# Kernel tuning notes

Measured on AMD Instinct MI355X. Metric: run time of the kernel, lower is better.

The kernel has to match this reference:

```python
import jax, jax.numpy as jnp
import numpy as np

COMMIT_WEIGHT = 0.25


def setup_inputs() -> dict:
    key = jax.random.key(0)
    k1, k2 = jax.random.split(key)
    B, D, T, K = 8, 512, 2048, 8192
    x = jax.random.normal(k1, (B, D, T), dtype=jnp.float32)
    codebook = jax.random.normal(k2, (K, D), dtype=jnp.float32)
    return {"x": x, "codebook": codebook}


def reference(x, codebook):
    # x: [B, D, T] channels-first; VQ operates on [B, T, D]
    xt = jnp.transpose(x, (0, 2, 1))  # [B, T, D]
    x2 = jnp.sum(xt * xt, axis=-1, keepdims=True)          # [B, T, 1]
    e2 = jnp.sum(codebook * codebook, axis=-1)             # [K]
    xe = jnp.einsum('btd,kd->btk', xt, codebook)           # [B, T, K] (dominant GEMM)
    dists = x2 - 2.0 * xe + e2                             # [B, T, K]
    indices = jnp.argmin(dists, axis=-1)                   # [B, T] int
    quantized = codebook[indices]                          # [B, T, D] gather
    # commitment loss: ||sg(q) - x||^2 mean
    commit_loss = COMMIT_WEIGHT * jnp.mean(
        (jax.lax.stop_gradient(quantized) - xt) ** 2)
    # straight-through estimator
    quantized = xt + jax.lax.stop_gradient(quantized - xt)
    quantized = jnp.transpose(quantized, (0, 2, 1))        # back to [B, D, T]
    return quantized, indices, commit_loss
```

## Files before the change

kernel.cpp:

```cpp
#include <hip/hip_runtime.h>
#include <cstdint>
#include <cstddef>

#define B_   8
#define D_   512
#define T_   2048
#define K_   8192
#define BT_  (B_ * T_)
#define NQ_  ((size_t)B_ * D_ * T_)

typedef _Float16 f16x8 __attribute__((ext_vector_type(8)));
typedef _Float16 f16x4 __attribute__((ext_vector_type(4)));
typedef float    f32x4 __attribute__((ext_vector_type(4)));
typedef unsigned long long u64;
typedef unsigned int u32;

#define WS_SLOTS_OFF    0
#define WS_FIDX_OFF     393216
#define WS_PART_OFF     458752
#define WS_E2_OFF       460800
#define WS_XH_OFF       524288
#define WS_XL_OFF       (WS_XH_OFF + 16777216)
#define WS_CH_OFF       (WS_XL_OFF + 16777216)
#define WS_NEEDED       ((size_t)WS_CH_OFF + 8388608)

__device__ __forceinline__ void gload_lds16(const void* g, void* l) {
    __builtin_amdgcn_global_load_lds(
        (const __attribute__((address_space(1))) void*)g,
        (__attribute__((address_space(3))) void*)l, 16, 0, 0);
}

__device__ __forceinline__ u32 fkey(float f) {
    u32 u = __float_as_uint(f);
    u ^= (u32)((int)u >> 31) | 0x80000000u;
    return u;
}
__device__ __forceinline__ u64 umin64(u64 a, u64 b) { return a < b ? a : b; }
__device__ __forceinline__ u64 umax64(u64 a, u64 b) { return a > b ? a : b; }

__global__ __launch_bounds__(256) void k_prepcb(const float* __restrict__ cb,
                                                _Float16* __restrict__ ch,
                                                float* __restrict__ e2) {
    const int wid = threadIdx.x >> 6, lane = threadIdx.x & 63;
    const int row = blockIdx.x * 4 + wid;
    const float4* src = (const float4*)(cb + (size_t)row * D_ + lane * 8);
    float4 a = src[0], b = src[1];
    f16x8 h;
    h[0] = (_Float16)a.x; h[1] = (_Float16)a.y;
    h[2] = (_Float16)a.z; h[3] = (_Float16)a.w;
    h[4] = (_Float16)b.x; h[5] = (_Float16)b.y;
    h[6] = (_Float16)b.z; h[7] = (_Float16)b.w;
    *(f16x8*)(ch + (size_t)row * D_ + lane * 8) = h;
    float s = a.x * a.x;
    s = fmaf(a.y, a.y, s); s = fmaf(a.z, a.z, s); s = fmaf(a.w, a.w, s);
    s = fmaf(b.x, b.x, s); s = fmaf(b.y, b.y, s);
    s = fmaf(b.z, b.z, s); s = fmaf(b.w, b.w, s);
#pragma unroll
    for (int st = 1; st < 64; st <<= 1) s += __shfl_xor(s, st);
    if (lane == 0) e2[row] = s;
}

__global__ __launch_bounds__(256) void k_e2(const float* __restrict__ cb,
                                            float* __restrict__ e2) {
    int k = blockIdx.x * 256 + threadIdx.x;
    const float4* row = (const float4*)(cb + (size_t)k * D_);
    float s = 0.f;
#pragma unroll 4
    for (int i = 0; i < D_ / 4; ++i) {
        float4 v = row[i];
        s = fmaf(v.x, v.x, s); s = fmaf(v.y, v.y, s);
        s = fmaf(v.z, v.z, s); s = fmaf(v.w, v.w, s);
    }
    e2[k] = s;
}

__global__ __launch_bounds__(256) void k_splitx(const float* __restrict__ x,
                                                _Float16* __restrict__ xh,
                                                _Float16* __restrict__ xl) {
    int b  = blockIdx.z;
    int d0 = blockIdx.y * 64;
    int t0 = blockIdx.x * 64;
    int dl = threadIdx.x & 63;
    int tq = threadIdx.x >> 6;
    const float* px = x + ((size_t)b * D_ + (d0 + dl)) * T_ + t0 + tq * 16;
#pragma unroll
    for (int i = 0; i < 4; ++i) {
        float4 v = *(const float4*)(px + i * 4);
#pragma unroll
        for (int j = 0; j < 4; ++j) {
            float vv = (j == 0) ? v.x : (j == 1) ? v.y : (j == 2) ? v.z : v.w;
            _Float16 h = (_Float16)vv;
            float lo = vv - (float)h;
            _Float16 l = (_Float16)lo;
            size_t row = (size_t)b * T_ + t0 + tq * 16 + i * 4 + j;
            xh[row * D_ + d0 + dl] = h;
            xl[row * D_ + d0 + dl] = l;
        }
    }
}

__global__ __launch_bounds__(512, 2)
void k_hi_argmin(const _Float16* __restrict__ xh, const _Float16* __restrict__ ch,
                 const float* __restrict__ e2, u64* __restrict__ slots) {
    __shared__ char smem[131072];
    __shared__ u32 stop[256][2][2];
    __shared__ float e2s[1024];

    const int tid = threadIdx.x;
    const int xcd = blockIdx.x & 7;
    const int bi  = blockIdx.x >> 3;
    const int m_  = bi >> 3;
    const int nblk = bi & 7;
    const int mbase  = (xcd * 8 + m_) * 256;
    const int nstart = nblk * 1024;

    const int lane = tid & 63;
    const int wid  = tid >> 6;
    const int wr = wid & 3, wc = wid >> 2;
    const int lr = lane & 15, lg = lane >> 4;

    {
        u32* p = (u32*)stop;
        p[tid] = ~0u; p[tid + 512] = ~0u;
        *(float2*)&e2s[tid * 2] = *(const float2*)&e2[nstart + tid * 2];
    }
    __syncthreads();

    const bool isA = wid < 4;
    const int q8 = lane >> 3;
    const int u8 = (lane & 7) ^ q8;
    const int srow2 = (u8 >> 2) & 1;
    const int sslot = u8 & 3;
    const char* gs0 = isA
        ? (const char*)xh + (size_t)(mbase  + (wid & 3) * 64 + 2 * q8 + srow2) * 1024
              + sslot * 16
        : (const char*)ch + (size_t)(nstart + (wid & 3) * 64 + 2 * q8 + srow2) * 1024
              + sslot * 16;
    const int ldsbase = (isA ? 0 : 16384) + (wid & 3) * 4096;

#define STAGE2(g, i0) do {                                                   \
        char* lb_ = smem + ((g) & 3) * 32768 + ldsbase;                      \
        const char* gs_ = gs0 + (isA ? 0 : (size_t)((g) >> 4) * 262144)      \
                          + ((g) & 15) * 64;                                 \
        gload_lds16(gs_ + (size_t)(i0) * 16384, lb_ + (i0) * 1024);          \
        gload_lds16(gs_ + (size_t)((i0) + 1) * 16384, lb_ + ((i0) + 1) * 1024); \
    } while (0)

    const int lrh = lr >> 1;
    const int swz16 = ((lg + 4 * (lr & 1)) ^ lrh) * 16;
    const int aoff0 = (wr * 32 + lrh) * 128 + swz16;
    const int boff0 = 16384 + (wc * 64 + lrh) * 128 + swz16;

    u32 top2a[16], top2b[16];
#pragma unroll
    for (int s = 0; s < 16; ++s) { top2a[s] = ~0u; top2b[s] = ~0u; }

    f32x4 acc[4][8];
#pragma unroll
    for (int m = 0; m < 4; ++m)
#pragma unroll
        for (int n = 0; n < 8; ++n)
            acc[m][n] = (f32x4){0.f, 0.f, 0.f, 0.f};

    auto epilogue = [&](int ns) {
        float e2v[8];
#pragma unroll
        for (int n = 0; n < 8; ++n)
            e2v[n] = 0.5f * e2s[ns * 256 + wc * 128 + n * 16 + lr];
        const u32 base10 = ((u32)ns << 8) | ((u32)wc << 7) | (u32)lr;
#pragma unroll
        for (int m = 0; m < 4; ++m) {
#pragma unroll
            for (int j = 0; j < 4; ++j) {
                const int s = m * 4 + j;
                u32 t1 = top2a[s], t2 = top2b[s];
#pragma unroll
                for (int n = 0; n < 8; ++n) {
                    float d = fmaxf(e2v[n] - acc[m][n][j], 1.0f);
                    u32 p = (__float_as_uint(d) & 0xFFFFFC00u) | (base10 + ((u32)n << 4));
                    u32 mx = t1 > p ? t1 : p;
                    t1 = t1 < p ? t1 : p;
                    t2 = t2 < mx ? t2 : mx;
                }
                top2a[s] = t1; top2b[s] = t2;
            }
        }
#pragma unroll
        for (int m = 0; m < 4; ++m)
#pragma unroll
            for (int n = 0; n < 8; ++n)
                acc[m][n] = (f32x4){0.f, 0.f, 0.f, 0.f};
    };

#define MFMA16(AF, BF, NOFF)                                                 \
        __builtin_amdgcn_s_setprio(1);                                       \
        _Pragma("unroll")                                                    \
        for (int m = 0; m < 4; ++m)                                          \
            _Pragma("unroll")                                                \
            for (int n = 0; n < 4; ++n)                                      \
                acc[m][(NOFF) + n] = __builtin_amdgcn_mfma_f32_16x16x32_f16( \
                    AF[m], BF[n], acc[m][(NOFF) + n], 0, 0, 0);              \
        __builtin_amdgcn_s_setprio(0);

#define SB __builtin_amdgcn_sched_barrier(0)

    STAGE2(0, 0); STAGE2(0, 2);
    STAGE2(1, 0); STAGE2(1, 2);
    STAGE2(2, 0); STAGE2(2, 2);
    asm volatile("s_waitcnt vmcnt(8)" ::: "memory");
    __builtin_amdgcn_s_barrier();
    SB;

#pragma unroll 1
    for (int s = 0; s < 64; ++s) {
        const char* base = smem + (s & 3) * 32768;
        f16x8 af[4], bf[4], bg[4];

#pragma unroll
        for (int m = 0; m < 4; ++m)
            af[m] = *(const f16x8*)(base + aoff0 + m * 1024);
#pragma unroll
        for (int n = 0; n < 4; ++n)
            bf[n] = *(const f16x8*)(base + boff0 + n * 1024);
        if (s < 61) STAGE2(s + 3, 0);
        SB;
        MFMA16(af, bf, 0)
        SB;
#pragma unroll
        for (int n = 0; n < 4; ++n)
            bg[n] = *(const f16x8*)(base + boff0 + (4 + n) * 1024);
        if (s < 61) STAGE2(s + 3, 2);
        SB;
        MFMA16(af, bg, 4)
        SB;

        if (s < 61)       asm volatile("s_waitcnt vmcnt(8)" ::: "memory");
        else if (s == 61) asm volatile("s_waitcnt vmcnt(4)" ::: "memory");
        else              asm volatile("s_waitcnt vmcnt(0)" ::: "memory");
        asm volatile("s_waitcnt lgkmcnt(0)" ::: "memory");
        SB;
        __builtin_amdgcn_s_barrier();
        SB;
        if ((s & 15) == 15) epilogue(s >> 4);
    }
#undef STAGE2
#undef MFMA16
#undef SB

#pragma unroll
    for (int m = 0; m < 4; ++m) {
#pragma unroll
        for (int j = 0; j < 4; ++j) {
            const int s = m * 4 + j;
            u32 t1 = top2a[s], t2 = top2b[s];
#pragma unroll
            for (int st = 1; st < 16; st <<= 1) {
                u32 o1 = __shfl_xor(t1, st);
                u32 o2 = __shfl_xor(t2, st);
                u32 mx = t1 > o1 ? t1 : o1;
                u32 sel = t1 < o1 ? t2 : o2;
                u32 n2 = mx < sel ? mx : sel;
                t1 = t1 < o1 ? t1 : o1;
                t2 = t2 < n2 ? t2 : n2;
            }
            if (lr == 0) {
                int ql = wr * 64 + m * 16 + lg * 4 + j;
                stop[ql][wc][0] = t1; stop[ql][wc][1] = t2;
            }
        }
    }

    __syncthreads();
    if (tid < 256) {
        u32 a1 = stop[tid][0][0], a2 = stop[tid][0][1];
        u32 b1 = stop[tid][1][0], b2 = stop[tid][1][1];
        u32 f1 = a1 < b1 ? a1 : b1;
        u32 mx = a1 > b1 ? a1 : b1;
        u32 sel = a1 < b1 ? a2 : b2;
        u32 f2 = mx < sel ? mx : sel;
        int q = mbase + tid;
        u64 p1 = ((u64)(f1 & 0xFFFFFC00u) << 32) | (u32)(nstart + (f1 & 0x3FFu));
        u64 p2 = ((u64)(f2 & 0xFFFFFC00u) << 32) | (u32)(nstart + (f2 & 0x3FFu));
        u64* As = slots + q;
        u64* Bs = slots + BT_ + q;
        u64* Cs = slots + 2 * BT_ + q;
        u64 old = atomicMin(As, p1);
        u64 v = umax64(old, p1);
        old = atomicMin(Bs, v);
        u64 v2 = umax64(old, v);
        atomicMin(Cs, v2);
        old = atomicMin(Bs, p2);
        v = umax64(old, p2);
        atomicMin(Cs, v);
    }
}

__global__ __launch_bounds__(256)
void k_rescore(const _Float16* __restrict__ xh, const _Float16* __restrict__ xl,
               const float* __restrict__ cb, const float* __restrict__ e2,
               const u64* __restrict__ slots,
               u32* __restrict__ final_idx, float* __restrict__ out_idx) {
    const int wid = threadIdx.x >> 6, lane = threadIdx.x & 63;
    const int q = blockIdx.x * 4 + wid;
    u64 a = slots[q], b = slots[BT_ + q], c = slots[2 * BT_ + q];
    u32 i1 = (u32)a, i2 = (u32)b, i3 = (u32)c;
    float d1 = __uint_as_float((u32)(a >> 32));
    float d2 = __uint_as_float((u32)(b >> 32));
    u32 win = i1;
    if (!(d2 - d1 > 0.75f)) {
        float xr[8];
        f16x8 hv = *(const f16x8*)(xh + (size_t)q * D_ + lane * 8);
        f16x8 lv = *(const f16x8*)(xl + (size_t)q * D_ + lane * 8);
#pragma unroll
        for (int i = 0; i < 8; ++i) xr[i] = (float)hv[i] + (float)lv[i];
        u32 idxs[3] = {i1, i2, i3};
        float key[3];
#pragma unroll 1
        for (int cnd = 0; cnd < 3; ++cnd) {
            const float4* cr = (const float4*)(cb + (size_t)idxs[cnd] * D_ + lane * 8);
            float4 c0 = cr[0], c1 = cr[1];
            float s = xr[0] * c0.x;
            s = fmaf(xr[1], c0.y, s); s = fmaf(xr[2], c0.z, s); s = fmaf(xr[3], c0.w, s);
            s = fmaf(xr[4], c1.x, s); s = fmaf(xr[5], c1.y, s);
            s = fmaf(xr[6], c1.z, s); s = fmaf(xr[7], c1.w, s);
#pragma unroll
            for (int st = 1; st < 64; st <<= 1) s += __shfl_xor(s, st);
            key[cnd] = e2[idxs[cnd]] - 2.f * s;
        }
        float bk = key[0]; win = idxs[0];
#pragma unroll
        for (int cnd = 1; cnd < 3; ++cnd) {
            if (key[cnd] < bk || (key[cnd] == bk && idxs[cnd] < win)) {
                bk = key[cnd]; win = idxs[cnd];
            }
        }
    }
    if (lane == 0) { final_idx[q] = win; out_idx[q] = (float)win; }
}

#define MB 64
#define NB 64
#define KC 32
#define FNSPLIT 2
#define KPER (K_ / FNSPLIT)
__global__ __launch_bounds__(256, 2)
void k_argmin_f32(const float* __restrict__ x, const float* __restrict__ cb,
                  const float* __restrict__ e2, u64* __restrict__ slots) {
    __shared__ float xs[KC][MB + 4];
    __shared__ float es[KC][NB + 4];
    __shared__ u64 red[MB];
    const int tid = threadIdx.x;
    const int tx = tid & 15, ty = tid >> 4;
    const int rowtile = blockIdx.x;
    const int b = rowtile >> 5;
    const int tbase = (rowtile & 31) * MB;
    const int nstart = blockIdx.y * KPER;
    if (tid < MB) red[tid] = ~0ull;
    float bestv[4]; int besti[4];
#pragma unroll
    for (int i = 0; i < 4; ++i) { bestv[i] = 3.4e38f; besti[i] = 0; }
    const int sm = tid & 63, sg = tid >> 6;
    const float* xbase = x + (size_t)b * D_ * T_ + (tbase + sm);
    for (int nb = 0; nb < KPER; nb += NB) {
        float acc[4][4];
#pragma unroll
        for (int i = 0; i < 4; ++i)
#pragma unroll
            for (int j = 0; j < 4; ++j) acc[i][j] = 0.f;
        for (int kc = 0; kc < D_; kc += KC) {
            __syncthreads();
#pragma unroll
            for (int r = 0; r < 8; ++r) {
                int dd = sg * 8 + r;
                xs[dd][sm] = xbase[(size_t)(kc + dd) * T_];
            }
            const float* crow = cb + (size_t)(nstart + nb + sm) * D_ + kc + sg * 8;
            float4 c0 = *(const float4*)(crow);
            float4 c1 = *(const float4*)(crow + 4);
            es[sg * 8 + 0][sm] = c0.x; es[sg * 8 + 1][sm] = c0.y;
            es[sg * 8 + 2][sm] = c0.z; es[sg * 8 + 3][sm] = c0.w;
            es[sg * 8 + 4][sm] = c1.x; es[sg * 8 + 5][sm] = c1.y;
            es[sg * 8 + 6][sm] = c1.z; es[sg * 8 + 7][sm] = c1.w;
            __syncthreads();
#pragma unroll
            for (int dd = 0; dd < KC; ++dd) {
                float4 a = *(const float4*)&xs[dd][tx * 4];
                float4 e = *(const float4*)&es[dd][ty * 4];
                acc[0][0] = fmaf(a.x, e.x, acc[0][0]); acc[0][1] = fmaf(a.x, e.y, acc[0][1]);
                acc[0][2] = fmaf(a.x, e.z, acc[0][2]); acc[0][3] = fmaf(a.x, e.w, acc[0][3]);
                acc[1][0] = fmaf(a.y, e.x, acc[1][0]); acc[1][1] = fmaf(a.y, e.y, acc[1][1]);
                acc[1][2] = fmaf(a.y, e.z, acc[1][2]); acc[1][3] = fmaf(a.y, e.w, acc[1][3]);
                acc[2][0] = fmaf(a.z, e.x, acc[2][0]); acc[2][1] = fmaf(a.z, e.y, acc[2][1]);
                acc[2][2] = fmaf(a.z, e.z, acc[2][2]); acc[2][3] = fmaf(a.z, e.w, acc[2][3]);
                acc[3][0] = fmaf(a.w, e.x, acc[3][0]); acc[3][1] = fmaf(a.w, e.y, acc[3][1]);
                acc[3][2] = fmaf(a.w, e.z, acc[3][2]); acc[3][3] = fmaf(a.w, e.w, acc[3][3]);
            }
        }
#pragma unroll
        for (int j = 0; j < 4; ++j) {
            int c = nstart + nb + ty * 4 + j;
            float ec = e2[c];
#pragma unroll
            for (int i = 0; i < 4; ++i) {
                float dist = fmaf(-2.f, acc[i][j], ec);
                if (dist < bestv[i]) { bestv[i] = dist; besti[i] = c; }
            }
        }
    }
    __syncthreads();
#pragma unroll
    for (int i = 0; i < 4; ++i) {
        u64 p = ((u64)fkey(bestv[i]) << 32) | (u32)besti[i];
        atomicMin(&red[tx * 4 + i], p);
    }
    __syncthreads();
    if (tid < MB) atomicMin(&slots[b * T_ + tbase + tid], red[tid]);
}

__global__ __launch_bounds__(256)
void k_finalize(const u64* __restrict__ slots,
                u32* __restrict__ final_idx, float* __restrict__ out_idx) {
    int q = blockIdx.x * 256 + threadIdx.x;
    u32 idx = (u32)slots[q];
    final_idx[q] = idx;
    out_idx[q] = (float)idx;
}

__global__ __launch_bounds__(256)
void k_gather(const float* __restrict__ x, const float* __restrict__ cb,
              const u32* __restrict__ final_idx,
              float* __restrict__ out_q, float* __restrict__ out_loss) {
    int tid = threadIdx.x;
    int btg = blockIdx.x * 256 + tid;
    int b = btg >> 11, t = btg & (T_ - 1);
    int dch = blockIdx.y;
    u32 idx = final_idx[btg];
    const float* crow = cb + (size_t)idx * D_;
    size_t xoff = (size_t)b * D_ * T_ + t;
    float ls = 0.f;
#pragma unroll 4
    for (int dd = 0; dd < 64; ++dd) {
        int d = dch * 64 + dd;
        float q = crow[d];
        size_t o = xoff + (size_t)d * T_;
        float xv = x[o];
        out_q[o] = q;
        float df = q - xv;
        ls = fmaf(df, df, ls);
    }
    __shared__ float rs[256];
    rs[tid] = ls;
    __syncthreads();
    for (int s = 128; s > 0; s >>= 1) {
        if (tid < s) rs[tid] += rs[tid + s];
        __syncthreads();
    }
    if (tid == 0) atomicAdd(out_loss, 0.25f * rs[0] / (float)NQ_);
}

extern "C" void kernel_launch(void* const* d_in, const int* in_sizes, int n_in,
                              void* d_out, int out_size, void* d_ws, size_t ws_size,
                              hipStream_t stream) {
    const float* x  = (const float*)d_in[0];
    const float* cb = (const float*)d_in[1];

    float* out_q    = (float*)d_out;
    float* out_idx  = out_q + NQ_;
    float* out_loss = out_idx + BT_;

    char* ws = (char*)d_ws;
    u64* slots = (u64*)(ws + WS_SLOTS_OFF);
    u32* fidx = (u32*)(ws + WS_FIDX_OFF);
    float* e2 = (float*)(ws + WS_E2_OFF);

    hipMemsetAsync(slots, 0xFF, (size_t)3 * BT_ * 8, stream);
    hipMemsetAsync(out_loss, 0, sizeof(float), stream);

    if (ws_size >= WS_NEEDED) {
        _Float16* xhp = (_Float16*)(ws + WS_XH_OFF);
        _Float16* xlp = (_Float16*)(ws + WS_XL_OFF);
        _Float16* chp = (_Float16*)(ws + WS_CH_OFF);
        k_prepcb<<<dim3(K_ / 4), dim3(256), 0, stream>>>(cb, chp, e2);
        k_splitx<<<dim3(T_ / 64, D_ / 64, B_), dim3(256), 0, stream>>>(x, xhp, xlp);
        k_hi_argmin<<<dim3(512), dim3(512), 0, stream>>>(xhp, chp, e2, slots);
        k_rescore<<<dim3(BT_ / 4), dim3(256), 0, stream>>>(xhp, xlp, cb, e2, slots,
                                                           fidx, out_idx);
    } else {
        k_e2<<<dim3(K_ / 256), dim3(256), 0, stream>>>(cb, e2);
        k_argmin_f32<<<dim3(BT_ / MB, FNSPLIT), dim3(256), 0, stream>>>(x, cb, e2, slots);
        k_finalize<<<dim3(BT_ / 256), dim3(256), 0, stream>>>(slots, fidx, out_idx);
    }

    k_gather<<<dim3(BT_ / 256, D_ / 64), dim3(256), 0, stream>>>(x, cb, fidx,
                                                                 out_q, out_loss);
}
```

Before: 200.6 us.

## Use 4-wave blocks with 128x128 per-wave tiles and triple-buffered LDS in argmin GEMM

The fp16 distance GEMM kernel drops from 8 waves to 4 waves per block, each wave now computing a 128-row by 128-column tile (8x8 MFMA accumulators) instead of 64x128. This raises register-level reuse of A fragments per LDS read. LDS staging goes from four stages to three, shrinking shared memory to 96KB. The cost is twice the accumulator registers per wave, lower occupancy (launch bounds 256,1), fewer waves to hide latency, and the removal of the MFMA priority hints.

```diff
diff --git a/kernel.cpp b/kernel.cpp
--- a/kernel.cpp
+++ b/kernel.cpp
@@ -99,10 +99,10 @@
     }
 }
 
-__global__ __launch_bounds__(512, 2)
+__global__ __launch_bounds__(256, 1)
 void k_hi_argmin(const _Float16* __restrict__ xh, const _Float16* __restrict__ ch,
                  const float* __restrict__ e2, u64* __restrict__ slots) {
-    __shared__ char smem[131072];
+    __shared__ char smem[98304];
     __shared__ u32 stop[256][2][2];
     __shared__ float e2s[1024];
 
@@ -116,48 +116,50 @@
 
     const int lane = tid & 63;
     const int wid  = tid >> 6;
-    const int wr = wid & 3, wc = wid >> 2;
+    const int wr = wid & 1, wc = wid >> 1;
     const int lr = lane & 15, lg = lane >> 4;
 
     {
         u32* p = (u32*)stop;
-        p[tid] = ~0u; p[tid + 512] = ~0u;
-        *(float2*)&e2s[tid * 2] = *(const float2*)&e2[nstart + tid * 2];
+        p[tid] = ~0u; p[tid + 256] = ~0u; p[tid + 512] = ~0u; p[tid + 768] = ~0u;
+        *(float4*)&e2s[tid * 4] = *(const float4*)&e2[nstart + tid * 4];
     }
     __syncthreads();
 
-    const bool isA = wid < 4;
+    const bool isA = wid < 2;
+    const int half = wid & 1;
     const int q8 = lane >> 3;
     const int u8 = (lane & 7) ^ q8;
     const int srow2 = (u8 >> 2) & 1;
     const int sslot = u8 & 3;
     const char* gs0 = isA
-        ? (const char*)xh + (size_t)(mbase  + (wid & 3) * 64 + 2 * q8 + srow2) * 1024
+        ? (const char*)xh + (size_t)(mbase  + half * 128 + 2 * q8 + srow2) * 1024
               + sslot * 16
-        : (const char*)ch + (size_t)(nstart + (wid & 3) * 64 + 2 * q8 + srow2) * 1024
+        : (const char*)ch + (size_t)(nstart + half * 128 + 2 * q8 + srow2) * 1024
               + sslot * 16;
-    const int ldsbase = (isA ? 0 : 16384) + (wid & 3) * 4096;
-
-#define STAGE2(g, i0) do {                                                   \
-        char* lb_ = smem + ((g) & 3) * 32768 + ldsbase;                      \
+    const int ldsbase = (isA ? 0 : 16384) + half * 8192;
+
+#define STAGE4(g, i0) do {                                                   \
+        char* lb_ = smem + ((g) % 3) * 32768 + ldsbase;                      \
         const char* gs_ = gs0 + (isA ? 0 : (size_t)((g) >> 4) * 262144)      \
                           + ((g) & 15) * 64;                                 \
-        gload_lds16(gs_ + (size_t)(i0) * 16384, lb_ + (i0) * 1024);          \
-        gload_lds16(gs_ + (size_t)((i0) + 1) * 16384, lb_ + ((i0) + 1) * 1024); \
+        _Pragma("unroll")                                                    \
+        for (int i_ = (i0); i_ < (i0) + 4; ++i_)                             \
+            gload_lds16(gs_ + (size_t)i_ * 16384, lb_ + i_ * 1024);          \
     } while (0)
 
     const int lrh = lr >> 1;
     const int swz16 = ((lg + 4 * (lr & 1)) ^ lrh) * 16;
-    const int aoff0 = (wr * 32 + lrh) * 128 + swz16;
+    const int aoff0 = (wr * 64 + lrh) * 128 + swz16;
     const int boff0 = 16384 + (wc * 64 + lrh) * 128 + swz16;
 
-    u32 top2a[16], top2b[16];
-#pragma unroll
-    for (int s = 0; s < 16; ++s) { top2a[s] = ~0u; top2b[s] = ~0u; }
-
-    f32x4 acc[4][8];
-#pragma unroll
-    for (int m = 0; m < 4; ++m)
+    u32 top2a[32], top2b[32];
+#pragma unroll
+    for (int s = 0; s < 32; ++s) { top2a[s] = ~0u; top2b[s] = ~0u; }
+
+    f32x4 acc[8][8];
+#pragma unroll
+    for (int m = 0; m < 8; ++m)
 #pragma unroll
         for (int n = 0; n < 8; ++n)
             acc[m][n] = (f32x4){0.f, 0.f, 0.f, 0.f};
@@ -169,7 +171,7 @@
             e2v[n] = 0.5f * e2s[ns * 256 + wc * 128 + n * 16 + lr];
         const u32 base10 = ((u32)ns << 8) | ((u32)wc << 7) | (u32)lr;
 #pragma unroll
-        for (int m = 0; m < 4; ++m) {
+        for (int m = 0; m < 8; ++m) {
 #pragma unroll
             for (int j = 0; j < 4; ++j) {
                 const int s = m * 4 + j;
@@ -186,69 +188,65 @@
             }
         }
 #pragma unroll
-        for (int m = 0; m < 4; ++m)
+        for (int m = 0; m < 8; ++m)
 #pragma unroll
             for (int n = 0; n < 8; ++n)
                 acc[m][n] = (f32x4){0.f, 0.f, 0.f, 0.f};
     };
 
-#define MFMA16(AF, BF, NOFF)                                                 \
-        __builtin_amdgcn_s_setprio(1);                                       \
+#define MFMA32(BF, NOFF)                                                     \
         _Pragma("unroll")                                                    \
-        for (int m = 0; m < 4; ++m)                                          \
+        for (int m = 0; m < 8; ++m)                                          \
             _Pragma("unroll")                                                \
             for (int n = 0; n < 4; ++n)                                      \
                 acc[m][(NOFF) + n] = __builtin_amdgcn_mfma_f32_16x16x32_f16( \
-                    AF[m], BF[n], acc[m][(NOFF) + n], 0, 0, 0);              \
-        __builtin_amdgcn_s_setprio(0);
+                    af[m], BF[n], acc[m][(NOFF) + n], 0, 0, 0);
 
 #define SB __builtin_amdgcn_sched_barrier(0)
 
-    STAGE2(0, 0); STAGE2(0, 2);
-    STAGE2(1, 0); STAGE2(1, 2);
-    STAGE2(2, 0); STAGE2(2, 2);
+    STAGE4(0, 0); STAGE4(0, 4);
+    STAGE4(1, 0); STAGE4(1, 4);
     asm volatile("s_waitcnt vmcnt(8)" ::: "memory");
     __builtin_amdgcn_s_barrier();
     SB;
 
 #pragma unroll 1
     for (int s = 0; s < 64; ++s) {
-        const char* base = smem + (s & 3) * 32768;
-        f16x8 af[4], bf[4], bg[4];
-
-#pragma unroll
-        for (int m = 0; m < 4; ++m)
+        const char* base = smem + (s % 3) * 32768;
+        f16x8 af[8], bf[4], bg[4];
+
+#pragma unroll
+        for (int m = 0; m < 8; ++m)
             af[m] = *(const f16x8*)(base + aoff0 + m * 1024);
 #pragma unroll
         for (int n = 0; n < 4; ++n)
             bf[n] = *(const f16x8*)(base + boff0 + n * 1024);
-        if (s < 61) STAGE2(s + 3, 0);
-        SB;
-        MFMA16(af, bf, 0)
+        if (s < 62) STAGE4(s + 2, 0);
+        SB;
+        MFMA32(bf, 0)
         SB;
 #pragma unroll
         for (int n = 0; n < 4; ++n)
             bg[n] = *(const f16x8*)(base + boff0 + (4 + n) * 1024);
-        if (s < 61) STAGE2(s + 3, 2);
-        SB;
-        MFMA16(af, bg, 4)
-        SB;
-
-        if (s < 61)       asm volatile("s_waitcnt vmcnt(8)" ::: "memory");
-        else if (s == 61) asm volatile("s_waitcnt vmcnt(4)" ::: "memory");
-        else              asm volatile("s_waitcnt vmcnt(0)" ::: "memory");
+        if (s < 62) STAGE4(s + 2, 4);
+        SB;
+        MFMA32(bg, 4)
+        SB;
+
+        if (s < 62) asm volatile("s_waitcnt vmcnt(8)" ::: "memory");
+        else        asm volatile("s_waitcnt vmcnt(0)" ::: "memory");
         asm volatile("s_waitcnt lgkmcnt(0)" ::: "memory");
         SB;
         __builtin_amdgcn_s_barrier();
         SB;
         if ((s & 15) == 15) epilogue(s >> 4);
     }
-#undef STAGE2
-#undef MFMA16
+#undef STAGE4
+#undef MFMA32
 #undef SB
 
 #pragma unroll
-    for (int m = 0; m < 4; ++m) {
+    for (int m = 0; m < 8; ++m) {
 #pragma unroll
         for (int j = 0; j < 4; ++j) {
             const int s = m * 4 + j;
@@ -264,14 +262,14 @@
                 t2 = t2 < n2 ? t2 : n2;
             }
             if (lr == 0) {
-                int ql = wr * 64 + m * 16 + lg * 4 + j;
+                int ql = wr * 128 + m * 16 + lg * 4 + j;
                 stop[ql][wc][0] = t1; stop[ql][wc][1] = t2;
             }
         }
     }
 
     __syncthreads();
-    if (tid < 256) {
+    {
         u32 a1 = stop[tid][0][0], a2 = stop[tid][0][1];
         u32 b1 = stop[tid][1][0], b2 = stop[tid][1][1];
         u32 f1 = a1 < b1 ? a1 : b1;
@@ -482,7 +480,7 @@
         _Float16* chp = (_Float16*)(ws + WS_CH_OFF);
         k_prepcb<<<dim3(K_ / 4), dim3(256), 0, stream>>>(cb, chp, e2);
         k_splitx<<<dim3(T_ / 64, D_ / 64, B_), dim3(256), 0, stream>>>(x, xhp, xlp);
-        k_hi_argmin<<<dim3(512), dim3(512), 0, stream>>>(xhp, chp, e2, slots);
+        k_hi_argmin<<<dim3(512), dim3(256), 0, stream>>>(xhp, chp, e2, slots);
         k_rescore<<<dim3(BT_ / 4), dim3(256), 0, stream>>>(xhp, xlp, cb, e2, slots,
                                                            fidx, out_idx);
     } else {
```

After: 593.1 us. +195.6%, slower.
